# Kernel tuning notes

Measured on AMD Instinct MI355X. Metric: run time of the kernel, lower is better.

## Reference

```python
import jax, jax.numpy as jnp
import numpy as np

B, S, E, H = 8, 2048, 256, 8
LN_EPS = 1e-5


def setup_inputs() -> dict:
    key = jax.random.key(0)
    ks = jax.random.split(key, 5)
    x = jax.random.normal(ks[0], (B, S, E), dtype=jnp.float32)
    Wq = jax.random.normal(ks[1], (E, E), dtype=jnp.float32) * 0.02
    Wk = jax.random.normal(ks[2], (E, E), dtype=jnp.float32) * 0.02
    Wv = jax.random.normal(ks[3], (E, E), dtype=jnp.float32) * 0.02
    bias_table = jax.random.normal(ks[4], (2 * S - 1, H), dtype=jnp.float32) * 0.02
    ln_gamma = jnp.ones((E,), dtype=jnp.float32)
    ln_beta = jnp.zeros((E,), dtype=jnp.float32)
    return {"x": x, "Wq": Wq, "Wk": Wk, "Wv": Wv,
            "bias_table": bias_table, "ln_gamma": ln_gamma, "ln_beta": ln_beta}


def reference(x, Wq, Wk, Wv, bias_table, ln_gamma, ln_beta):
    b, s, e = x.shape
    h = bias_table.shape[1]
    d = e // h
    scale = e ** (-0.5)  # note: original scales by emb_size**-0.5, not head_dim

    # torch nn.Linear(bias=False): y = x @ W.T
    q = (x @ Wq.T).reshape(b, s, h, d).transpose(0, 2, 1, 3)  # [b,h,s,d]
    k = (x @ Wk.T).reshape(b, s, h, d).transpose(0, 2, 1, 3)
    v = (x @ Wv.T).reshape(b, s, h, d).transpose(0, 2, 1, 3)

    # full attention matrix (the chunked torch loop computes exactly this)
    attn = jax.nn.softmax(jnp.einsum('bhqd,bhkd->bhqk', q, k) * scale, axis=-1)

    # relative bias: index[i,j] = i - j + (s-1); added AFTER softmax (faithful)
    idx = jnp.arange(s)[:, None] - jnp.arange(s)[None, :] + (s - 1)  # [s,s]
    rel_bias = bias_table[idx].transpose(2, 0, 1)  # [h,s,s]
    attn = attn + rel_bias[None]

    out = jnp.einsum('bhqk,bhkd->bhqd', attn, v)
    out = out.transpose(0, 2, 1, 3).reshape(b, s, e)

    # LayerNorm over last dim
    mu = jnp.mean(out, axis=-1, keepdims=True)
    var = jnp.var(out, axis=-1, keepdims=True)
    out = (out - mu) * jax.lax.rsqrt(var + LN_EPS) * ln_gamma + ln_beta
    return out
```

## Files before the change

### kernel.cpp

```cpp
#include <hip/hip_runtime.h>
#include <math.h>

typedef unsigned short u16;
typedef unsigned int u32;
typedef __attribute__((ext_vector_type(8))) short short8;
typedef __attribute__((ext_vector_type(16))) float floatx16;

constexpr int CB = 8;
constexpr int CS = 2048;
constexpr int CE = 256;
constexpr int CH = 8;
constexpr int CD = 32;
constexpr float CLN_EPS = 1e-5f;
constexpr float QSC = 0.0625f * 1.44269504088896341f;

constexpr int QP = 40;
constexpr int VP = 72;
constexpr int XP = 264;
constexpr int BSPAN = 2175;
constexpr int BP4 = 2180;

__device__ inline u32 fbits(float f) { union { float f; u32 u; } c; c.f = f; return c.u; }
__device__ inline u32 pack2(float a, float b) {
  return __builtin_amdgcn_perm(fbits(b) + 0x8000u, fbits(a) + 0x8000u, 0x07060302u);
}
__device__ inline u16 bf1(float a) { return (u16)((fbits(a) + 0x8000u) >> 16); }
__device__ inline short8 ld8(const u16* p) {
  union { uint4 q; short8 v; } c; c.q = *(const uint4*)p; return c.v;
}

#if __has_builtin(__builtin_amdgcn_permlane32_swap)
__device__ inline void swap32(u32& a, u32& b) {
  typedef __attribute__((ext_vector_type(2))) unsigned int uint2v;
  uint2v r = __builtin_amdgcn_permlane32_swap(a, b, false, false);
  a = r[0]; b = r[1];
}
#else
__device__ inline void swap32(u32& a, u32& b) {
  int hi = (threadIdx.x >> 5) & 1;
  u32 sa = (u32)__shfl_xor((int)a, 32);
  u32 sb = (u32)__shfl_xor((int)b, 32);
  u32 na = hi ? sb : a;
  u32 nb = hi ? b : sa;
  a = na; b = nb;
}
#endif

__global__ __launch_bounds__(256) void cvt_w_kernel(const float* __restrict__ Wq,
                                                    const float* __restrict__ Wk,
                                                    const float* __restrict__ Wv,
                                                    u16* __restrict__ Wb) {
  int gid = blockIdx.x * 256 + threadIdx.x;
  int which = gid >> 14;
  int off = (gid & 16383) * 4;
  const float* W = (which == 0) ? Wq : (which == 1) ? Wk : Wv;
  float4 f = *(const float4*)&W[off];
  uint2 o; o.x = pack2(f.x, f.y); o.y = pack2(f.z, f.w);
  *(uint2*)&Wb[(size_t)which * CE * CE + off] = o;
}

__global__ __launch_bounds__(256, 3) void qkv_mfma_kernel(
    const float* __restrict__ x, const u16* __restrict__ Wb,
    u16* __restrict__ qb, u16* __restrict__ kb, u16* __restrict__ vb) {
  __shared__ __attribute__((aligned(16))) u16 Xs[32 * XP];
  const int m0 = blockIdx.x * 32;
  const int nh = blockIdx.y;
  const int tid = threadIdx.x;
  const int lane = tid & 63, wv = tid >> 6;
  const int lm = lane & 31, lg = lane >> 5;

#pragma unroll
  for (int it = 0; it < 8; ++it) {
    int c = tid + 256 * it;
    int row = c >> 6, f4 = c & 63;
    float4 f = *(const float4*)&x[(size_t)(m0 + row) * CE + f4 * 4];
    uint2 o; o.x = pack2(f.x, f.y); o.y = pack2(f.z, f.w);
    *(uint2*)&Xs[row * XP + f4 * 4] = o;
  }
  __syncthreads();

  short8 xf[16];
#pragma unroll
  for (int kt = 0; kt < 16; ++kt) xf[kt] = ld8(&Xs[lm * XP + kt * 16 + lg * 8]);

  const int sg = m0 + lm;
  const int bI = sg >> 11, sI = sg & (CS - 1);

  for (int j = 0; j < 3; ++j) {
    int t = nh * 12 + wv * 3 + j;
    int which = t >> 3;
    int nc = (t & 7) * 32;
    int h = nc >> 5;
    const u16* Wsrc = Wb + (size_t)which * CE * CE;
    floatx16 acc;
#pragma unroll
    for (int i = 0; i < 16; ++i) acc[i] = 0.f;
    {
      short8 wf[8];
#pragma unroll
      for (int kt = 0; kt < 8; ++kt)
        wf[kt] = ld8(&Wsrc[(size_t)(nc + lm) * CE + kt * 16 + lg * 8]);
#pragma unroll
      for (int kt = 0; kt < 8; ++kt)
        acc = __builtin_amdgcn_mfma_f32_32x32x16_bf16(wf[kt], xf[kt], acc, 0, 0, 0);
    }
    {
      short8 wf[8];
#pragma unroll
      for (int kt = 0; kt < 8; ++kt)
        wf[kt] = ld8(&Wsrc[(size_t)(nc + lm) * CE + (kt + 8) * 16 + lg * 8]);
#pragma unroll
      for (int kt = 0; kt < 8; ++kt)
        acc = __builtin_amdgcn_mfma_f32_32x32x16_bf16(wf[kt], xf[kt + 8], acc, 0, 0, 0);
    }
    if (which < 2) {
      u16* dst = which ? kb : qb;
      float scl = which ? 1.0f : QSC;
      u32 D[8];
#pragma unroll
      for (int g = 0; g < 8; ++g)
        D[g] = pack2(acc[2 * g] * scl, acc[2 * g + 1] * scl);
      swap32(D[0], D[2]); swap32(D[1], D[3]);
      swap32(D[4], D[6]); swap32(D[5], D[7]);
      size_t base = (((size_t)bI * CH + h) * CS + sI) * CD;
      uint4 U0; U0.x = D[0]; U0.y = D[1]; U0.z = D[2]; U0.w = D[3];
      uint4 U1; U1.x = D[4]; U1.y = D[5]; U1.z = D[6]; U1.w = D[7];
      *(uint4*)&dst[base + 8 * lg] = U0;
      *(uint4*)&dst[base + 16 + 8 * lg] = U1;
    } else {
#pragma unroll
      for (int r = 0; r < 16; ++r) {
        int d = (r & 3) + 8 * (r >> 2) + 4 * lg;
        vb[(((size_t)bI * CH + h) * CD + d) * CS + sI] = bf1(acc[r]);
      }
    }
  }
}

__global__ __launch_bounds__(256, 3) void attn_mfma_kernel(
    const u16* __restrict__ qm, const u16* __restrict__ km,
    const u16* __restrict__ vm, const float* __restrict__ table,
    float* __restrict__ out) {
  __shared__ __attribute__((aligned(16))) u16 Ks[2][64 * QP];
  __shared__ __attribute__((aligned(16))) u16 Vt[2][32 * VP];
  __shared__ __attribute__((aligned(16))) u16 Bs[4 * BP4];

  const int q0 = blockIdx.x * 128;
  const int bh = blockIdx.y;
  const int b = bh >> 3, h = bh & 7;
  const int tid = threadIdx.x;
  const int lane = tid & 63, wv = tid >> 6;
  const int lm = lane & 31, lg = lane >> 5;
  const u16* qbp = qm + (size_t)bh * CS * CD;
  const u16* kbp = km + (size_t)bh * CS * CD;
  const u16* vbp = vm + (size_t)bh * CD * CS;

  for (int i = tid; i < BSPAN; i += 256) {
    u16 bv = bf1(table[(size_t)(q0 + BSPAN - 1 - i) * CH + h]);
#pragma unroll
    for (int c = 0; c < 4; ++c)
      if (i >= c) Bs[c * BP4 + i - c] = bv;
  }

  const int qrow = wv * 32 + lm;
  const u16* qp = qbp + (size_t)(q0 + qrow) * CD;
  short8 qa0 = ld8(qp + lg * 8);
  short8 qa1 = ld8(qp + 16 + lg * 8);

  const int krow = tid >> 2, kch = tid & 3;
  const int vrow = tid >> 3, vch = tid & 7;
  uint4 kreg = *(const uint4*)&kbp[(size_t)krow * CD + kch * 8];
  uint4 vreg = *(const uint4*)&vbp[(size_t)vrow * CS + vch * 8];

  floatx16 acc_e, acc_b;
#pragma unroll
  for (int i = 0; i < 16; ++i) { acc_e[i] = 0.f; acc_b[i] = 0.f; }
  float l = 0.f;

  for (int k0 = 0; k0 < CS; k0 += 64) {
    const int p = (k0 >> 6) & 1;
    *(uint4*)&Ks[p][krow * QP + kch * 8] = kreg;
    *(uint4*)&Vt[p][vrow * VP + vch * 8] = vreg;
    if (k0 + 64 < CS) {
      kreg = *(const uint4*)&kbp[(size_t)(k0 + 64 + krow) * CD + kch * 8];
      vreg = *(const uint4*)&vbp[(size_t)vrow * CS + (k0 + 64) + vch * 8];
    }
    __syncthreads();

    floatx16 sc0, sc1;
#pragma unroll
    for (int i = 0; i < 16; ++i) { sc0[i] = 0.f; sc1[i] = 0.f; }
    {
      short8 a00 = ld8(&Ks[p][lm * QP + lg * 8]);
      short8 a01 = ld8(&Ks[p][lm * QP + 16 + lg * 8]);
      short8 a10 = ld8(&Ks[p][(32 + lm) * QP + lg * 8]);
      short8 a11 = ld8(&Ks[p][(32 + lm) * QP + 16 + lg * 8]);
      sc0 = __builtin_amdgcn_mfma_f32_32x32x16_bf16(a00, qa0, sc0, 0, 0, 0);
      sc0 = __builtin_amdgcn_mfma_f32_32x32x16_bf16(a01, qa1, sc0, 0, 0, 0);
      sc1 = __builtin_amdgcn_mfma_f32_32x32x16_bf16(a10, qa0, sc1, 0, 0, 0);
      sc1 = __builtin_amdgcn_mfma_f32_32x32x16_bf16(a11, qa1, sc1, 0, 0, 0);
    }

#pragma unroll
    for (int ct = 0; ct < 2; ++ct) {
      floatx16& sc = ct ? sc1 : sc0;
      u32 P[8];
#pragma unroll
      for (int g = 0; g < 8; ++g) {
        float e0 = __builtin_amdgcn_exp2f(sc[2 * g]);
        float e1 = __builtin_amdgcn_exp2f(sc[2 * g + 1]);
        l += e0 + e1;
        P[g] = pack2(e0, e1);
      }
      swap32(P[0], P[2]); swap32(P[1], P[3]);
      swap32(P[4], P[6]); swap32(P[5], P[7]);
      union { u32 u[4]; short8 v; } B0, B1;
      B0.u[0] = P[0]; B0.u[1] = P[1]; B0.u[2] = P[2]; B0.u[3] = P[3];
      B1.u[0] = P[4]; B1.u[1] = P[5]; B1.u[2] = P[6]; B1.u[3] = P[7];
      short8 va0 = ld8(&Vt[p][lm * VP + ct * 32 + lg * 8]);
      short8 va1 = ld8(&Vt[p][lm * VP + ct * 32 + 16 + lg * 8]);
      acc_e = __builtin_amdgcn_mfma_f32_32x32x16_bf16(va0, B0.v, acc_e, 0, 0, 0);
      acc_e = __builtin_amdgcn_mfma_f32_32x32x16_bf16(va1, B1.v, acc_e, 0, 0, 0);
      union { u32 u[4]; short8 v; } Bb0, Bb1;
      {
        int i00 = 127 - qrow + k0 + ct * 32 + lg * 8;
        int c = i00 & 3;
        const u16* src = &Bs[c * BP4 + (i00 - c)];
        *(uint2*)&Bb0.u[0] = *(const uint2*)src;
        *(uint2*)&Bb0.u[2] = *(const uint2*)(src + 4);
        int i01 = i00 + 16;
        int c1 = i01 & 3;
        const u16* src1 = &Bs[c1 * BP4 + (i01 - c1)];
        *(uint2*)&Bb1.u[0] = *(const uint2*)src1;
        *(uint2*)&Bb1.u[2] = *(const uint2*)(src1 + 4);
      }
      acc_b = __builtin_amdgcn_mfma_f32_32x32x16_bf16(va0, Bb0.v, acc_b, 0, 0, 0);
      acc_b = __builtin_amdgcn_mfma_f32_32x32x16_bf16(va1, Bb1.v, acc_b, 0, 0, 0);
    }
  }

  l += __shfl_xor(l, 32);
  float rl = __builtin_amdgcn_rcpf(l);
  size_t ob = ((size_t)b * CS + q0 + qrow) * CE + h * CD;
#pragma unroll
  for (int g = 0; g < 4; ++g) {
    float4 r4;
    r4.x = acc_e[4 * g + 0] * rl + acc_b[4 * g + 0];
    r4.y = acc_e[4 * g + 1] * rl + acc_b[4 * g + 1];
    r4.z = acc_e[4 * g + 2] * rl + acc_b[4 * g + 2];
    r4.w = acc_e[4 * g + 3] * rl + acc_b[4 * g + 3];
    *(float4*)&out[ob + 8 * g + 4 * lg] = r4;
  }
}

__global__ __launch_bounds__(256) void ln_kernel(float* __restrict__ io,
                                                 const float* __restrict__ gamma,
                                                 const float* __restrict__ beta) {
  int tid = threadIdx.x;
  size_t row = (size_t)blockIdx.x * 4 + (tid >> 6);
  int c = (tid & 63) * 4;
  float4 v = *(const float4*)&io[row * CE + c];
  float s1 = v.x + v.y + v.z + v.w;
  float s2 = v.x * v.x + v.y * v.y + v.z * v.z + v.w * v.w;
#pragma unroll
  for (int off = 1; off < 64; off <<= 1) {
    s1 += __shfl_xor(s1, off);
    s2 += __shfl_xor(s2, off);
  }
  float mu = s1 * (1.0f / CE);
  float var = s2 * (1.0f / CE) - mu * mu;
  float rs = rsqrtf(var + CLN_EPS);
  float4 g = *(const float4*)&gamma[c];
  float4 be = *(const float4*)&beta[c];
  float4 o;
  o.x = (v.x - mu) * rs * g.x + be.x;
  o.y = (v.y - mu) * rs * g.y + be.y;
  o.z = (v.z - mu) * rs * g.z + be.z;
  o.w = (v.w - mu) * rs * g.w + be.w;
  *(float4*)&io[row * CE + c] = o;
}

extern "C" void kernel_launch(void* const* d_in, const int* in_sizes, int n_in,
                              void* d_out, int out_size, void* d_ws, size_t ws_size,
                              hipStream_t stream) {
  (void)in_sizes; (void)n_in; (void)out_size; (void)ws_size;
  const float* x          = (const float*)d_in[0];
  const float* Wq         = (const float*)d_in[1];
  const float* Wk         = (const float*)d_in[2];
  const float* Wv         = (const float*)d_in[3];
  const float* bias_table = (const float*)d_in[4];
  const float* gamma      = (const float*)d_in[5];
  const float* beta       = (const float*)d_in[6];
  float* out = (float*)d_out;

  u16* ws = (u16*)d_ws;
  u16* Wb = ws;
  u16* qb = Wb + 3 * CE * CE;
  u16* kb = qb + (size_t)CB * CH * CS * CD;
  u16* vb = kb + (size_t)CB * CH * CS * CD;

  cvt_w_kernel<<<dim3(192), dim3(256), 0, stream>>>(Wq, Wk, Wv, Wb);
  qkv_mfma_kernel<<<dim3(512, 2), dim3(256), 0, stream>>>(x, Wb, qb, kb, vb);
  attn_mfma_kernel<<<dim3(CS / 128, CB * CH), dim3(256), 0, stream>>>(qb, kb, vb, bias_table, out);
  ln_kernel<<<dim3(CB * CS / 4), dim3(256), 0, stream>>>(out, gamma, beta);
}
```

Before: 179.3 us.

## Precompute reversed bias table in global memory, read it directly in attention

A new prep kernel builds a bf16 reversed relative-bias table per head, with 8 shifted copies so that every lane's 8-element slice is 16-byte aligned. The attention kernel drops its per-block LDS bias staging loop and the four-way shifted LDS copies, and instead issues aligned uint4 global loads for the bias fragment each k-step. Freeing that LDS allows launch bounds to rise to 4 blocks per CU. The cost is extra global/L2 traffic inside the main loop and one small extra kernel launch.

```diff
diff --git a/kernel.cpp b/kernel.cpp
--- a/kernel.cpp
+++ b/kernel.cpp
@@ -17,8 +17,7 @@
 constexpr int QP = 40;
 constexpr int VP = 72;
 constexpr int XP = 264;
-constexpr int BSPAN = 2175;
-constexpr int BP4 = 2180;
+constexpr int RST = 4104;
 
 __device__ inline u32 fbits(float f) { union { float f; u32 u; } c; c.f = f; return c.u; }
 __device__ inline u32 pack2(float a, float b) {
@@ -59,6 +58,22 @@
   *(uint2*)&Wb[(size_t)which * CE * CE + off] = o;
 }
 
+__global__ __launch_bounds__(256) void rev_prep_kernel(const float* __restrict__ table,
+                                                       u16* __restrict__ revg) {
+  int gid = blockIdx.x * 256 + threadIdx.x;
+  if (gid >= 64 * 513) return;
+  int g = gid / 513;
+  int j0 = (gid - g * 513) * 8;
+  int h = g >> 3, p = g & 7;
+  u16 vals[8];
+#pragma unroll
+  for (int t = 0; t < 8; ++t) {
+    int src = 4094 - (j0 + t + p);
+    vals[t] = (src >= 0) ? bf1(table[(size_t)src * CH + h]) : (u16)0;
+  }
+  *(uint4*)&revg[(size_t)g * RST + j0] = *(uint4*)vals;
+}
+
 __global__ __launch_bounds__(256, 3) void qkv_mfma_kernel(
     const float* __restrict__ x, const u16* __restrict__ Wb,
     u16* __restrict__ qb, u16* __restrict__ kb, u16* __restrict__ vb) {
@@ -137,13 +152,12 @@
   }
 }
 
-__global__ __launch_bounds__(256, 3) void attn_mfma_kernel(
+__global__ __launch_bounds__(256, 4) void attn_mfma_kernel(
     const u16* __restrict__ qm, const u16* __restrict__ km,
-    const u16* __restrict__ vm, const float* __restrict__ table,
+    const u16* __restrict__ vm, const u16* __restrict__ revg,
     float* __restrict__ out) {
   __shared__ __attribute__((aligned(16))) u16 Ks[2][64 * QP];
   __shared__ __attribute__((aligned(16))) u16 Vt[2][32 * VP];
-  __shared__ __attribute__((aligned(16))) u16 Bs[4 * BP4];
 
   const int q0 = blockIdx.x * 128;
   const int bh = blockIdx.y;
@@ -155,17 +169,14 @@
   const u16* kbp = km + (size_t)bh * CS * CD;
   const u16* vbp = vm + (size_t)bh * CD * CS;
 
-  for (int i = tid; i < BSPAN; i += 256) {
-    u16 bv = bf1(table[(size_t)(q0 + BSPAN - 1 - i) * CH + h]);
-#pragma unroll
-    for (int c = 0; c < 4; ++c)
-      if (i >= c) Bs[c * BP4 + i - c] = bv;
-  }
-
   const int qrow = wv * 32 + lm;
   const u16* qp = qbp + (size_t)(q0 + qrow) * CD;
   short8 qa0 = ld8(qp + lg * 8);
   short8 qa1 = ld8(qp + 16 + lg * 8);
+
+  const int Xb = 2047 - q0 - qrow + lg * 8;
+  const int pp = Xb & 7;
+  const u16* bp = revg + (size_t)(h * 8 + pp) * RST + (Xb - pp);
 
   const int krow = tid >> 2, kch = tid & 3;
   const int vrow = tid >> 3, vch = tid & 7;
@@ -185,6 +196,10 @@
       kreg = *(const uint4*)&kbp[(size_t)(k0 + 64 + krow) * CD + kch * 8];
       vreg = *(const uint4*)&vbp[(size_t)vrow * CS + (k0 + 64) + vch * 8];
     }
+    uint4 bu0 = *(const uint4*)&bp[k0];
+    uint4 bu1 = *(const uint4*)&bp[k0 + 16];
+    uint4 bu2 = *(const uint4*)&bp[k0 + 32];
+    uint4 bu3 = *(const uint4*)&bp[k0 + 48];
     __syncthreads();
 
     floatx16 sc0, sc1;
@@ -221,19 +236,9 @@
       short8 va1 = ld8(&Vt[p][lm * VP + ct * 32 + 16 + lg * 8]);
       acc_e = __builtin_amdgcn_mfma_f32_32x32x16_bf16(va0, B0.v, acc_e, 0, 0, 0);
       acc_e = __builtin_amdgcn_mfma_f32_32x32x16_bf16(va1, B1.v, acc_e, 0, 0, 0);
-      union { u32 u[4]; short8 v; } Bb0, Bb1;
-      {
-        int i00 = 127 - qrow + k0 + ct * 32 + lg * 8;
-        int c = i00 & 3;
-        const u16* src = &Bs[c * BP4 + (i00 - c)];
-        *(uint2*)&Bb0.u[0] = *(const uint2*)src;
-        *(uint2*)&Bb0.u[2] = *(const uint2*)(src + 4);
-        int i01 = i00 + 16;
-        int c1 = i01 & 3;
-        const u16* src1 = &Bs[c1 * BP4 + (i01 - c1)];
-        *(uint2*)&Bb1.u[0] = *(const uint2*)src1;
-        *(uint2*)&Bb1.u[2] = *(const uint2*)(src1 + 4);
-      }
+      union { uint4 q; short8 v; } Bb0, Bb1;
+      Bb0.q = ct ? bu2 : bu0;
+      Bb1.q = ct ? bu3 : bu1;
       acc_b = __builtin_amdgcn_mfma_f32_32x32x16_bf16(va0, Bb0.v, acc_b, 0, 0, 0);
       acc_b = __builtin_amdgcn_mfma_f32_32x32x16_bf16(va1, Bb1.v, acc_b, 0, 0, 0);
     }
@@ -298,9 +303,11 @@
   u16* qb = Wb + 3 * CE * CE;
   u16* kb = qb + (size_t)CB * CH * CS * CD;
   u16* vb = kb + (size_t)CB * CH * CS * CD;
+  u16* revg = vb + (size_t)CB * CH * CS * CD;
 
   cvt_w_kernel<<<dim3(192), dim3(256), 0, stream>>>(Wq, Wk, Wv, Wb);
+  rev_prep_kernel<<<dim3(129), dim3(256), 0, stream>>>(bias_table, revg);
   qkv_mfma_kernel<<<dim3(512, 2), dim3(256), 0, stream>>>(x, Wb, qb, kb, vb);
-  attn_mfma_kernel<<<dim3(CS / 128, CB * CH), dim3(256), 0, stream>>>(qb, kb, vb, bias_table, out);
+  attn_mfma_kernel<<<dim3(CS / 128, CB * CH), dim3(256), 0, stream>>>(qb, kb, vb, revg, out);
   ln_kernel<<<dim3(CB * CS / 4), dim3(256), 0, stream>>>(out, gamma, beta);
 }
```

Result: no change. 182.3 us (+1.6%).
